# Kernel optimization log

Hardware: AMD Instinct MI355X
Metric: run time of the kernel (lower is better)

Reference implementation:

```python
import jax, jax.numpy as jnp
import numpy as np

N = 4_194_304
DT = 1800.0   # dt_s (30-minute steps)
G = 0.76      # solar transmittance g
AZ = 41.3     # glazed area Az


def setup_inputs() -> dict:
    key = jax.random.key(0)
    ks = jax.random.split(key, 16)
    f32 = jnp.float32
    def pos(k, lo, hi):  # positive scalar param
        return jax.random.uniform(k, (), dtype=f32, minval=lo, maxval=hi)
    return {
        # RC parameters (physically positive)
        "R_ie": pos(ks[0], 0.5, 2.0),
        "R_ea": pos(ks[1], 0.5, 2.0),
        "C_in": pos(ks[2], 1e6, 5e6),
        "C_en": pos(ks[3], 1e7, 5e7),
        "a_sol_in": pos(ks[4], 0.1, 0.9),
        "a_sol_en": pos(ks[5], 0.1, 0.9),
        "a_int_in": pos(ks[6], 0.1, 0.9),
        "a_int_en": pos(ks[7], 0.1, 0.9),
        "Tin0": jax.random.uniform(ks[8], (), dtype=f32, minval=18.0, maxval=22.0),
        # driver time series
        "To": jax.random.normal(ks[9], (N,), dtype=f32) * 5.0 + 10.0,
        "Irr": jax.random.uniform(ks[10], (N,), dtype=f32, maxval=800.0),
        "Qint": jax.random.uniform(ks[11], (N,), dtype=f32, maxval=500.0),
        "Qah": jax.random.uniform(ks[12], (N,), dtype=f32, maxval=3000.0),
        "Ria": jax.random.uniform(ks[13], (N,), dtype=f32, minval=0.05, maxval=0.5),
    }


def _simulate(R_ie, R_ea, C_in, C_en, a_sol_in, a_sol_en, a_int_in, a_int_en,
              Tin0, To, Irr, Qint, Qah, Ria):
    dt = jnp.float32(DT)
    Ria_c = jnp.maximum(Ria, 1e-6)                      # (n,)
    # A matrix entries (A22 varies per step via Ria)
    A11 = -(1.0 / R_ea + 1.0 / R_ie) / C_en             # scalar
    A12 = (1.0 / R_ie) / C_en                           # scalar
    A21 = (1.0 / R_ie) / C_in                           # scalar
    A22 = -(1.0 / Ria_c + 1.0 / R_ie) / C_in            # (n,)
    # M = I - dt*A, closed-form 2x2 inverse via determinant
    M11 = 1.0 - dt * A11                                # scalar
    M12 = -dt * A12                                     # scalar
    M21 = -dt * A21                                     # scalar
    M22 = 1.0 - dt * A22                                # (n,)
    det = M11 * M22 - M12 * M21                         # (n,)
    # dt * B @ u, vectorized over all steps
    Qsol = (G * AZ) * Irr                               # (n,)
    bu0 = dt * (To / (C_en * R_ea) + (a_sol_en / C_en) * Qsol + (a_int_en / C_en) * Qint)
    bu1 = dt * (To / (C_in * Ria_c) + (a_sol_in / C_in) * Qsol + (a_int_in / C_in) * Qint + Qah / C_in)

    def step(x, inp):
        b0, b1, m22, d = inp
        r0 = x[0] + b0
        r1 = x[1] + b1
        xn0 = (m22 * r0 - M12 * r1) / d
        xn1 = (-M21 * r0 + M11 * r1) / d
        return jnp.stack([xn0, xn1]), xn1

    x0 = jnp.stack([Tin0, Tin0])
    _, Tin_seq = jax.lax.scan(step, x0, (bu0, bu1, M22, det))
    return Tin_seq                                      # (n,) indoor temps


def reference(R_ie, R_ea, C_in, C_en, a_sol_in, a_sol_en, a_int_in, a_int_en,
              Tin0, To, Irr, Qint, Qah, Ria):
    return _simulate(R_ie, R_ea, C_in, C_en, a_sol_in, a_sol_en, a_int_in, a_int_en,
                     Tin0, To, Irr, Qint, Qah, Ria)
```

## Files before the change

kernel.cpp:

```cpp
#include <hip/hip_runtime.h>

#define BLOCK 256
#define SPAN  2048
#define ITERS 2

struct Xf { float p, q, r, s, u, v; };

__device__ __forceinline__ Xf xf_id() {
    Xf t; t.p = 1.f; t.q = 0.f; t.r = 0.f; t.s = 1.f; t.u = 0.f; t.v = 0.f;
    return t;
}

__device__ __forceinline__ Xf xf_compose(const Xf& E, const Xf& L) {
    Xf o;
    o.p = L.p * E.p + L.q * E.r;
    o.q = L.p * E.q + L.q * E.s;
    o.r = L.r * E.p + L.s * E.r;
    o.s = L.r * E.q + L.s * E.s;
    o.u = L.p * E.u + L.q * E.v + L.u;
    o.v = L.r * E.u + L.s * E.v + L.v;
    return o;
}

struct Par {
    float M11, M12, M21, Kx;
    float c0, c1;
    float cTo0, cIrr0, cQi0;
    float cIrr1, cQi1;
};

__device__ __forceinline__ Par make_par(
    const float* pRie, const float* pRea, const float* pCin, const float* pCen,
    const float* pAsi, const float* pAse, const float* pAii, const float* pAie)
{
    const float dt = 1800.0f;
    const float GA = 0.76f * 41.3f;
    float R_ie = *pRie, R_ea = *pRea, C_in = *pCin, C_en = *pCen;
    float asi = *pAsi, ase = *pAse, aii = *pAii, aie = *pAie;
    Par P;
    float iRie = 1.0f / R_ie;
    P.M11 = 1.0f + dt * (1.0f / R_ea + iRie) / C_en;
    P.M12 = -(dt * iRie) / C_en;
    P.M21 = -(dt * iRie) / C_in;
    P.Kx  = P.M12 * P.M21;
    P.c1  = dt / C_in;
    P.c0  = 1.0f + P.c1 * iRie;
    P.cTo0  = dt / (C_en * R_ea);
    P.cIrr0 = dt * ase * GA / C_en;
    P.cQi0  = dt * aie / C_en;
    P.cIrr1 = dt * asi * GA / C_in;
    P.cQi1  = dt * aii / C_in;
    return P;
}

__device__ __forceinline__ Xf step_xf(const Par& P, float to, float ir, float qi,
                                      float qa, float ra,
                                      float* rRo, float* b0o, float* b1o)
{
    float rR  = __builtin_amdgcn_rcpf(fmaxf(ra, 1e-6f));
    float b0  = P.cTo0 * to + P.cIrr0 * ir + P.cQi0 * qi;
    float b1  = P.c1 * fmaf(to, rR, qa) + P.cIrr1 * ir + P.cQi1 * qi;
    float M22 = fmaf(P.c1, rR, P.c0);
    float det = fmaf(P.M11, M22, -P.Kx);
    float rd  = __builtin_amdgcn_rcpf(det);
    Xf T;
    T.p =  M22 * rd;
    T.q = -P.M12 * rd;
    T.r = -P.M21 * rd;
    T.s =  P.M11 * rd;
    T.u = T.p * b0 + T.q * b1;
    T.v = T.r * b0 + T.s * b1;
    if (rRo) { *rRo = rR; *b0o = b0; *b1o = b1; }
    return T;
}

__device__ __forceinline__ Xf shfl_down_xf(const Xf& v, int d) {
    Xf o;
    o.p = __shfl_down(v.p, d, 64);
    o.q = __shfl_down(v.q, d, 64);
    o.r = __shfl_down(v.r, d, 64);
    o.s = __shfl_down(v.s, d, 64);
    o.u = __shfl_down(v.u, d, 64);
    o.v = __shfl_down(v.v, d, 64);
    return o;
}
__device__ __forceinline__ Xf shfl_up_xf(const Xf& v, int d) {
    Xf o;
    o.p = __shfl_up(v.p, d, 64);
    o.q = __shfl_up(v.q, d, 64);
    o.r = __shfl_up(v.r, d, 64);
    o.s = __shfl_up(v.s, d, 64);
    o.u = __shfl_up(v.u, d, 64);
    o.v = __shfl_up(v.v, d, 64);
    return o;
}

__device__ __forceinline__ void sm6_store(float* b, const Xf& v) {
    b[0] = v.p; b[1] = v.q; b[2] = v.r; b[3] = v.s; b[4] = v.u; b[5] = v.v;
}
__device__ __forceinline__ Xf sm6_load(const float* b) {
    Xf v; v.p = b[0]; v.q = b[1]; v.r = b[2]; v.s = b[3]; v.u = b[4]; v.v = b[5];
    return v;
}

__device__ __forceinline__ void load4(
    const float* __restrict__ To, const float* __restrict__ Irr,
    const float* __restrict__ Qi, const float* __restrict__ Qa,
    const float* __restrict__ Ra, int gstep, int N,
    float* tox, float* irx, float* qix, float* qax, float* rax)
{
    if (gstep + 4 <= N) {
        float4 v;
        v = *(const float4*)(To  + gstep); tox[0]=v.x; tox[1]=v.y; tox[2]=v.z; tox[3]=v.w;
        v = *(const float4*)(Irr + gstep); irx[0]=v.x; irx[1]=v.y; irx[2]=v.z; irx[3]=v.w;
        v = *(const float4*)(Qi  + gstep); qix[0]=v.x; qix[1]=v.y; qix[2]=v.z; qix[3]=v.w;
        v = *(const float4*)(Qa  + gstep); qax[0]=v.x; qax[1]=v.y; qax[2]=v.z; qax[3]=v.w;
        v = *(const float4*)(Ra  + gstep); rax[0]=v.x; rax[1]=v.y; rax[2]=v.z; rax[3]=v.w;
    } else {
#pragma unroll
        for (int j = 0; j < 4; ++j) {
            int gi = gstep + j; bool val = gi < N;
            tox[j] = val ? To[gi]  : 0.f;
            irx[j] = val ? Irr[gi] : 0.f;
            qix[j] = val ? Qi[gi]  : 0.f;
            qax[j] = val ? Qa[gi]  : 0.f;
            rax[j] = val ? Ra[gi]  : 1.f;
        }
    }
}

__global__ __launch_bounds__(BLOCK, 8) void k_blocksum(
    const float* __restrict__ To, const float* __restrict__ Irr,
    const float* __restrict__ Qi, const float* __restrict__ Qa,
    const float* __restrict__ Ra,
    const float* pRie, const float* pRea, const float* pCin, const float* pCen,
    const float* pAsi, const float* pAse, const float* pAii, const float* pAie,
    Xf* __restrict__ blkX, int N)
{
    __shared__ float smW[4 * 6];
    const int t = threadIdx.x;
    const int lane = t & 63;
    const int w = t >> 6;
    const int blockBase = blockIdx.x * SPAN;
    Par P = make_par(pRie, pRea, pCin, pCen, pAsi, pAse, pAii, pAie);

    Xf blockAgg = xf_id();
#pragma unroll
    for (int iter = 0; iter < ITERS; ++iter) {
        const int gstep = blockBase + iter * 1024 + 4 * t;
        float tox[4], irx[4], qix[4], qax[4], rax[4];
        load4(To, Irr, Qi, Qa, Ra, gstep, N, tox, irx, qix, qax, rax);
        Xf v = xf_id();
#pragma unroll
        for (int j = 0; j < 4; ++j)
            if (gstep + j < N)
                v = xf_compose(v, step_xf(P, tox[j], irx[j], qix[j], qax[j], rax[j],
                                          nullptr, nullptr, nullptr));
#pragma unroll
        for (int d = 1; d < 64; d <<= 1) {
            Xf u = shfl_down_xf(v, d);
            v = xf_compose(v, u);
        }
        if (lane == 0) sm6_store(smW + w * 6, v);
        __syncthreads();
        if (t == 0) {
            Xf ia = sm6_load(smW + 0);
            ia = xf_compose(ia, sm6_load(smW + 6));
            ia = xf_compose(ia, sm6_load(smW + 12));
            ia = xf_compose(ia, sm6_load(smW + 18));
            blockAgg = xf_compose(blockAgg, ia);
        }
        __syncthreads();
    }
    if (t == 0) blkX[blockIdx.x] = blockAgg;
}

__device__ __forceinline__ void sm_store(float* sm, int i, const Xf& v) {
    float* b = sm + i * 7;
    b[0] = v.p; b[1] = v.q; b[2] = v.r; b[3] = v.s; b[4] = v.u; b[5] = v.v;
}
__device__ __forceinline__ Xf sm_load(const float* sm, int i) {
    const float* b = sm + i * 7;
    Xf v; v.p = b[0]; v.q = b[1]; v.r = b[2]; v.s = b[3]; v.u = b[4]; v.v = b[5];
    return v;
}
__device__ __forceinline__ Xf block_scan(Xf v, float* sm) {
    const int t = threadIdx.x;
    sm_store(sm, t, v);
    __syncthreads();
    for (int off = 1; off < BLOCK; off <<= 1) {
        Xf e;
        bool has = (t >= off);
        if (has) e = sm_load(sm, t - off);
        __syncthreads();
        if (has) { v = xf_compose(e, v); sm_store(sm, t, v); }
        __syncthreads();
    }
    return v;
}

__global__ __launch_bounds__(BLOCK) void k_mid(
    const Xf* __restrict__ blkX, float2* __restrict__ blkSt,
    const float* pTin0, int NB)
{
    const int t = threadIdx.x;
    const int ser = (NB + BLOCK - 1) / BLOCK;
    const int base = t * ser;
    Xf acc = xf_id();
    for (int j = 0; j < ser; ++j) {
        int i = base + j;
        if (i < NB) acc = xf_compose(acc, blkX[i]);
    }
    __shared__ float sm[BLOCK * 7];
    block_scan(acc, sm);
    Xf E = xf_id();
    if (t > 0) E = sm_load(sm, t - 1);
    float T0 = *pTin0;
    float x0 = (E.p + E.q) * T0 + E.u;
    float x1 = (E.r + E.s) * T0 + E.v;
    for (int j = 0; j < ser; ++j) {
        int i = base + j;
        if (i < NB) {
            blkSt[i] = make_float2(x0, x1);
            Xf T = blkX[i];
            float n0 = T.p * x0 + T.q * x1 + T.u;
            float n1 = T.r * x0 + T.s * x1 + T.v;
            x0 = n0; x1 = n1;
        }
    }
}

__global__ __launch_bounds__(BLOCK, 4) void k_emit(
    const float* __restrict__ To, const float* __restrict__ Irr,
    const float* __restrict__ Qi, const float* __restrict__ Qa,
    const float* __restrict__ Ra,
    const float* pRie, const float* pRea, const float* pCin, const float* pCen,
    const float* pAsi, const float* pAse, const float* pAii, const float* pAie,
    const float2* __restrict__ blkSt, float* __restrict__ out, int N)
{
    __shared__ float smW[4 * ITERS * 6];
    const int t = threadIdx.x;
    const int lane = t & 63;
    const int w = t >> 6;
    const int blockBase = blockIdx.x * SPAN;
    Par P = make_par(pRie, pRea, pCin, pCen, pAsi, pAse, pAii, pAie);

    float rRv[ITERS][4], b0v[ITERS][4], b1v[ITERS][4];
    Xf sc[ITERS];

#pragma unroll
    for (int iter = 0; iter < ITERS; ++iter) {
        const int gstep = blockBase + iter * 1024 + 4 * t;
        float tox[4], irx[4], qix[4], qax[4], rax[4];
        load4(To, Irr, Qi, Qa, Ra, gstep, N, tox, irx, qix, qax, rax);
        Xf v = xf_id();
#pragma unroll
        for (int j = 0; j < 4; ++j) {
            Xf T = step_xf(P, tox[j], irx[j], qix[j], qax[j], rax[j],
                           &rRv[iter][j], &b0v[iter][j], &b1v[iter][j]);
            if (gstep + j < N) v = xf_compose(v, T);
        }
#pragma unroll
        for (int d = 1; d < 64; d <<= 1) {
            Xf u = shfl_up_xf(v, d);
            if (lane >= d) v = xf_compose(u, v);
        }
        sc[iter] = v;
        if (lane == 63) sm6_store(smW + (w * ITERS + iter) * 6, v);
    }
    __syncthreads();

    float2 B = blkSt[blockIdx.x];
    float Sx = B.x, Sy = B.y;
#pragma unroll
    for (int iter = 0; iter < ITERS; ++iter) {
        Xf Wpre = xf_id();
        for (int ww = 0; ww < w; ++ww)
            Wpre = xf_compose(Wpre, sm6_load(smW + (ww * ITERS + iter) * 6));
        Xf lex = shfl_up_xf(sc[iter], 1);
        if (lane == 0) lex = xf_id();
        Xf E = xf_compose(Wpre, lex);
        float x0 = E.p * Sx + E.q * Sy + E.u;
        float x1 = E.r * Sx + E.s * Sy + E.v;

        const int gstep = blockBase + iter * 1024 + 4 * t;
        float ov[4];
#pragma unroll
        for (int j = 0; j < 4; ++j) {
            float rR  = rRv[iter][j];
            float M22 = fmaf(P.c1, rR, P.c0);
            float det = fmaf(P.M11, M22, -P.Kx);
            float rd  = __builtin_amdgcn_rcpf(det);
            float r0 = x0 + b0v[iter][j];
            float r1 = x1 + b1v[iter][j];
            float n0 = (M22 * r0 - P.M12 * r1) * rd;
            float n1 = (P.M11 * r1 - P.M21 * r0) * rd;
            x0 = n0; x1 = n1; ov[j] = n1;
        }
        if (gstep + 4 <= N) {
            float4 o; o.x = ov[0]; o.y = ov[1]; o.z = ov[2]; o.w = ov[3];
            *(float4*)(out + gstep) = o;
        } else {
#pragma unroll
            for (int j = 0; j < 4; ++j) { int gi = gstep + j; if (gi < N) out[gi] = ov[j]; }
        }

        Xf A = sm6_load(smW + (0 * ITERS + iter) * 6);
        A = xf_compose(A, sm6_load(smW + (1 * ITERS + iter) * 6));
        A = xf_compose(A, sm6_load(smW + (2 * ITERS + iter) * 6));
        A = xf_compose(A, sm6_load(smW + (3 * ITERS + iter) * 6));
        float nSx = A.p * Sx + A.q * Sy + A.u;
        float nSy = A.r * Sx + A.s * Sy + A.v;
        Sx = nSx; Sy = nSy;
    }
}

extern "C" void kernel_launch(void* const* d_in, const int* in_sizes, int n_in,
                              void* d_out, int out_size, void* d_ws, size_t ws_size,
                              hipStream_t stream)
{
    (void)n_in; (void)out_size; (void)ws_size;
    const float* pRie = (const float*)d_in[0];
    const float* pRea = (const float*)d_in[1];
    const float* pCin = (const float*)d_in[2];
    const float* pCen = (const float*)d_in[3];
    const float* pAsi = (const float*)d_in[4];
    const float* pAse = (const float*)d_in[5];
    const float* pAii = (const float*)d_in[6];
    const float* pAie = (const float*)d_in[7];
    const float* pTin0 = (const float*)d_in[8];
    const float* To  = (const float*)d_in[9];
    const float* Irr = (const float*)d_in[10];
    const float* Qi  = (const float*)d_in[11];
    const float* Qa  = (const float*)d_in[12];
    const float* Ra  = (const float*)d_in[13];
    float* outp = (float*)d_out;
    int N = in_sizes[9];
    if (N <= 0) return;

    const int NB = (N + SPAN - 1) / SPAN;

    Xf* blkX = (Xf*)d_ws;
    size_t off = ((size_t)NB * sizeof(Xf) + 255) & ~(size_t)255;
    float2* blkSt = (float2*)((char*)d_ws + off);

    k_blocksum<<<NB, BLOCK, 0, stream>>>(To, Irr, Qi, Qa, Ra,
        pRie, pRea, pCin, pCen, pAsi, pAse, pAii, pAie, blkX, N);
    k_mid<<<1, BLOCK, 0, stream>>>(blkX, blkSt, pTin0, NB);
    k_emit<<<NB, BLOCK, 0, stream>>>(To, Irr, Qi, Qa, Ra,
        pRie, pRea, pCin, pCen, pAsi, pAse, pAii, pAie, blkSt, outp, N);
}
```

Measured before the change: 49.48 us.

## Remove middle scan kernel; each emit block reduces prior block aggregates itself

Removes the single-block k_mid launch. Each k_emit block now reduces all preceding block transforms from blkX, using per-thread serial composition plus a wave and cross-wave reduction, to get its starting state. k_blocksum also drops one of its per-iteration barriers by storing wave results for both iterations and combining them once. This trades a serial single-block kernel and one launch for redundant O(NB) reads and composes in every emit block.

```diff
diff --git a/kernel.cpp b/kernel.cpp
--- a/kernel.cpp
+++ b/kernel.cpp
@@ -137,14 +137,13 @@
     const float* pAsi, const float* pAse, const float* pAii, const float* pAie,
     Xf* __restrict__ blkX, int N)
 {
-    __shared__ float smW[4 * 6];
+    __shared__ float smW[4 * ITERS * 6];
     const int t = threadIdx.x;
     const int lane = t & 63;
     const int w = t >> 6;
     const int blockBase = blockIdx.x * SPAN;
     Par P = make_par(pRie, pRea, pCin, pCen, pAsi, pAse, pAii, pAie);
 
-    Xf blockAgg = xf_id();
 #pragma unroll
     for (int iter = 0; iter < ITERS; ++iter) {
         const int gstep = blockBase + iter * 1024 + 4 * t;
@@ -161,72 +160,16 @@
             Xf u = shfl_down_xf(v, d);
             v = xf_compose(v, u);
         }
-        if (lane == 0) sm6_store(smW + w * 6, v);
-        __syncthreads();
-        if (t == 0) {
-            Xf ia = sm6_load(smW + 0);
-            ia = xf_compose(ia, sm6_load(smW + 6));
-            ia = xf_compose(ia, sm6_load(smW + 12));
-            ia = xf_compose(ia, sm6_load(smW + 18));
-            blockAgg = xf_compose(blockAgg, ia);
-        }
-        __syncthreads();
-    }
-    if (t == 0) blkX[blockIdx.x] = blockAgg;
-}
-
-__device__ __forceinline__ void sm_store(float* sm, int i, const Xf& v) {
-    float* b = sm + i * 7;
-    b[0] = v.p; b[1] = v.q; b[2] = v.r; b[3] = v.s; b[4] = v.u; b[5] = v.v;
-}
-__device__ __forceinline__ Xf sm_load(const float* sm, int i) {
-    const float* b = sm + i * 7;
-    Xf v; v.p = b[0]; v.q = b[1]; v.r = b[2]; v.s = b[3]; v.u = b[4]; v.v = b[5];
-    return v;
-}
-__device__ __forceinline__ Xf block_scan(Xf v, float* sm) {
-    const int t = threadIdx.x;
-    sm_store(sm, t, v);
+        if (lane == 0) sm6_store(smW + (w * ITERS + iter) * 6, v);
+    }
     __syncthreads();
-    for (int off = 1; off < BLOCK; off <<= 1) {
-        Xf e;
-        bool has = (t >= off);
-        if (has) e = sm_load(sm, t - off);
-        __syncthreads();
-        if (has) { v = xf_compose(e, v); sm_store(sm, t, v); }
-        __syncthreads();
-    }
-    return v;
-}
-
-__global__ __launch_bounds__(BLOCK) void k_mid(
-    const Xf* __restrict__ blkX, float2* __restrict__ blkSt,
-    const float* pTin0, int NB)
-{
-    const int t = threadIdx.x;
-    const int ser = (NB + BLOCK - 1) / BLOCK;
-    const int base = t * ser;
-    Xf acc = xf_id();
-    for (int j = 0; j < ser; ++j) {
-        int i = base + j;
-        if (i < NB) acc = xf_compose(acc, blkX[i]);
-    }
-    __shared__ float sm[BLOCK * 7];
-    block_scan(acc, sm);
-    Xf E = xf_id();
-    if (t > 0) E = sm_load(sm, t - 1);
-    float T0 = *pTin0;
-    float x0 = (E.p + E.q) * T0 + E.u;
-    float x1 = (E.r + E.s) * T0 + E.v;
-    for (int j = 0; j < ser; ++j) {
-        int i = base + j;
-        if (i < NB) {
-            blkSt[i] = make_float2(x0, x1);
-            Xf T = blkX[i];
-            float n0 = T.p * x0 + T.q * x1 + T.u;
-            float n1 = T.r * x0 + T.s * x1 + T.v;
-            x0 = n0; x1 = n1;
-        }
+    if (t == 0) {
+        Xf acc = xf_id();
+#pragma unroll
+        for (int iter = 0; iter < ITERS; ++iter)
+            for (int ww = 0; ww < 4; ++ww)
+                acc = xf_compose(acc, sm6_load(smW + (ww * ITERS + iter) * 6));
+        blkX[blockIdx.x] = acc;
     }
 }
 
@@ -236,13 +179,17 @@
     const float* __restrict__ Ra,
     const float* pRie, const float* pRea, const float* pCin, const float* pCen,
     const float* pAsi, const float* pAse, const float* pAii, const float* pAie,
-    const float2* __restrict__ blkSt, float* __restrict__ out, int N)
+    const float* pTin0, const Xf* __restrict__ blkX,
+    float* __restrict__ out, int N, int NB)
 {
     __shared__ float smW[4 * ITERS * 6];
+    __shared__ float smSp[4 * 6];
+    __shared__ float smE[2];
     const int t = threadIdx.x;
     const int lane = t & 63;
     const int w = t >> 6;
-    const int blockBase = blockIdx.x * SPAN;
+    const int b = blockIdx.x;
+    const int blockBase = b * SPAN;
     Par P = make_par(pRie, pRea, pCin, pCen, pAsi, pAse, pAii, pAie);
 
     float rRv[ITERS][4], b0v[ITERS][4], b1v[ITERS][4];
@@ -268,10 +215,34 @@
         sc[iter] = v;
         if (lane == 63) sm6_store(smW + (w * ITERS + iter) * 6, v);
     }
+
+    {
+        const int SER = (NB + BLOCK - 1) / BLOCK;
+        Xf acc = xf_id();
+        for (int j = 0; j < SER; ++j) {
+            int idx = t * SER + j;
+            if (idx < b) acc = xf_compose(acc, blkX[idx]);
+        }
+#pragma unroll
+        for (int d = 1; d < 64; d <<= 1) {
+            Xf u = shfl_down_xf(acc, d);
+            acc = xf_compose(acc, u);
+        }
+        if (lane == 0) sm6_store(smSp + w * 6, acc);
+    }
     __syncthreads();
-
-    float2 B = blkSt[blockIdx.x];
-    float Sx = B.x, Sy = B.y;
+    if (t == 0) {
+        Xf A = sm6_load(smSp + 0);
+        A = xf_compose(A, sm6_load(smSp + 6));
+        A = xf_compose(A, sm6_load(smSp + 12));
+        A = xf_compose(A, sm6_load(smSp + 18));
+        float T0 = *pTin0;
+        smE[0] = (A.p + A.q) * T0 + A.u;
+        smE[1] = (A.r + A.s) * T0 + A.v;
+    }
+    __syncthreads();
+
+    float Sx = smE[0], Sy = smE[1];
 #pragma unroll
     for (int iter = 0; iter < ITERS; ++iter) {
         Xf Wpre = xf_id();
@@ -339,14 +310,11 @@
     if (N <= 0) return;
 
     const int NB = (N + SPAN - 1) / SPAN;
-
     Xf* blkX = (Xf*)d_ws;
-    size_t off = ((size_t)NB * sizeof(Xf) + 255) & ~(size_t)255;
-    float2* blkSt = (float2*)((char*)d_ws + off);
 
     k_blocksum<<<NB, BLOCK, 0, stream>>>(To, Irr, Qi, Qa, Ra,
         pRie, pRea, pCin, pCen, pAsi, pAse, pAii, pAie, blkX, N);
-    k_mid<<<1, BLOCK, 0, stream>>>(blkX, blkSt, pTin0, NB);
     k_emit<<<NB, BLOCK, 0, stream>>>(To, Irr, Qi, Qa, Ra,
-        pRie, pRea, pCin, pCen, pAsi, pAse, pAii, pAie, blkSt, outp, N);
-}
+        pRie, pRea, pCin, pCen, pAsi, pAse, pAii, pAie, pTin0, blkX,
+        outp, N, NB);
+}
```

Result: faster. 46.13 us (median of 2 runs) (-6.8%).
